# Kernel optimization log

Measured on AMD Instinct MI355X. Metric: run time of the kernel, lower is better.

## Reference

```python
import jax, jax.numpy as jnp
import numpy as np

EMBED_DIM = 1024
NUM_HEADS = 16
HEAD_DIM = EMBED_DIM // NUM_HEADS
MAX_LEN = 1000  # default in RelativePositionalEncoding
B, T = 4, 1024


def setup_inputs() -> dict:
    key = jax.random.key(0)
    ks = jax.random.split(key, 12)
    s = 0.02
    d = EMBED_DIM
    return {
        "query": jax.random.normal(ks[0], (B, T, d), jnp.float32),
        "key": jax.random.normal(ks[1], (B, T, d), jnp.float32),
        "value": jax.random.normal(ks[2], (B, T, d), jnp.float32),
        "Wq": jax.random.normal(ks[3], (d, d), jnp.float32) * s,
        "bq": jnp.zeros((d,), jnp.float32),
        "Wk": jax.random.normal(ks[4], (d, d), jnp.float32) * s,
        "bk": jnp.zeros((d,), jnp.float32),
        "Wv": jax.random.normal(ks[5], (d, d), jnp.float32) * s,
        "bv": jnp.zeros((d,), jnp.float32),
        "Wo": jax.random.normal(ks[6], (d, d), jnp.float32) * s,
        "bo": jnp.zeros((d,), jnp.float32),
        "rel_emb": jax.random.normal(ks[7], (2 * MAX_LEN - 1, HEAD_DIM), jnp.float32) * s,
    }


def reference(query, key, value, Wq, bq, Wk, bk, Wv, bv, Wo, bo, rel_emb):
    Bq, Tq, C = query.shape
    H, hd = NUM_HEADS, HEAD_DIM
    # projections -> [B, H, T, hd]
    q = (query @ Wq.T + bq).reshape(Bq, Tq, H, hd).transpose(0, 2, 1, 3)
    k = (key @ Wk.T + bk).reshape(Bq, Tq, H, hd).transpose(0, 2, 1, 3)
    v = (value @ Wv.T + bv).reshape(Bq, Tq, H, hd).transpose(0, 2, 1, 3)
    # content scores [B, H, T, T]
    attn_scores = jnp.einsum('bhtd,bhsd->bhts', q, k)
    # relative positional embedding gather: E[t, s] = rel_emb[clamp(s - t + max_len - 1)]
    pos = jnp.arange(Tq)
    idx = jnp.clip(pos[None, :] - pos[:, None] + MAX_LEN - 1, 0, 2 * MAX_LEN - 2)
    E = rel_emb[idx]  # [T, T, hd]
    # NOTE: original uses raw (unprojected) query reshaped into heads for rel-pos scores
    rpe_q = query.transpose(1, 0, 2).reshape(Tq, Bq * H, hd)  # [T, B*H, hd]
    rpe = jnp.einsum('tnd,tsd->nts', rpe_q, E).reshape(Bq, H, Tq, Tq)
    # faithful to original: divide by scale = hd**-0.5 (i.e. multiply by sqrt(hd))
    scale = hd ** (-0.5)
    attn = (attn_scores + rpe) / scale
    attn_weights = jax.nn.softmax(attn, axis=-1)
    out = jnp.einsum('bhts,bhsd->bhtd', attn_weights, v)
    out = out.transpose(0, 2, 1, 3).reshape(Bq, Tq, C)
    return out @ Wo.T + bo
```

## Files before the change

### kernel.cpp

```cpp
#include <hip/hip_runtime.h>
#include <math.h>

typedef _Float16 h16;
typedef __attribute__((ext_vector_type(8))) _Float16 half8;
typedef __attribute__((ext_vector_type(4))) float f32x4;

#define MFMA16(a, b, c) __builtin_amdgcn_mfma_f32_16x16x32_f16((a), (b), (c), 0, 0, 0)

__device__ __forceinline__ float ex2(float x) {
  return __builtin_amdgcn_exp2f(x);
}

template <bool A_F16>
__device__ __forceinline__ void gemm_body(const void* __restrict__ Ap,
                                          const float* __restrict__ Bt,
                                          const float* __restrict__ bias,
                                          void* __restrict__ outp, int mode) {
  __shared__ alignas(16) h16 As[128 * 32];
  __shared__ alignas(16) h16 Bs[128 * 32];
  const int tid = threadIdx.x;
  const int wave = tid >> 6;
  const int lane = tid & 63;
  const int wm = wave >> 1, wn = wave & 1;
  const int tm0 = blockIdx.x * 128, tn0 = blockIdx.y * 128;
  const int lrow = lane & 15;
  const int kq = lane >> 4;

  f32x4 acc[4][4];
#pragma unroll
  for (int i = 0; i < 4; ++i)
#pragma unroll
    for (int j = 0; j < 4; ++j) acc[i][j] = (f32x4){0.f, 0.f, 0.f, 0.f};

  for (int k0 = 0; k0 < 1024; k0 += 32) {
    __syncthreads();
#pragma unroll
    for (int rep = 0; rep < 2; ++rep) {
      const int idx = rep * 256 + tid;
      const int row = idx >> 2;
      const int c8 = (idx & 3) * 8;
      if (A_F16) {
        *(half8*)(As + row * 32 + c8) = *(const half8*)(
            (const h16*)Ap + (size_t)(tm0 + row) * 1024 + k0 + c8);
      } else {
        const float* ga =
            (const float*)Ap + (size_t)(tm0 + row) * 1024 + k0 + c8;
        float4 f0 = *(const float4*)ga;
        float4 f1 = *(const float4*)(ga + 4);
        half8 s;
        s[0] = (h16)f0.x; s[1] = (h16)f0.y; s[2] = (h16)f0.z; s[3] = (h16)f0.w;
        s[4] = (h16)f1.x; s[5] = (h16)f1.y; s[6] = (h16)f1.z; s[7] = (h16)f1.w;
        *(half8*)(As + row * 32 + c8) = s;
      }
      const float* gb = Bt + (size_t)(tn0 + row) * 1024 + k0 + c8;
      float4 g0 = *(const float4*)gb;
      float4 g1 = *(const float4*)(gb + 4);
      half8 sb;
      sb[0] = (h16)g0.x; sb[1] = (h16)g0.y; sb[2] = (h16)g0.z; sb[3] = (h16)g0.w;
      sb[4] = (h16)g1.x; sb[5] = (h16)g1.y; sb[6] = (h16)g1.z; sb[7] = (h16)g1.w;
      *(half8*)(Bs + row * 32 + c8) = sb;
    }
    __syncthreads();
    half8 af[4], bf[4];
#pragma unroll
    for (int i = 0; i < 4; ++i)
      af[i] = *(const half8*)(As + (wm * 64 + i * 16 + lrow) * 32 + kq * 8);
#pragma unroll
    for (int j = 0; j < 4; ++j)
      bf[j] = *(const half8*)(Bs + (wn * 64 + j * 16 + lrow) * 32 + kq * 8);
#pragma unroll
    for (int i = 0; i < 4; ++i)
#pragma unroll
      for (int j = 0; j < 4; ++j) acc[i][j] = MFMA16(af[i], bf[j], acc[i][j]);
  }

#pragma unroll
  for (int j = 0; j < 4; ++j) {
    const int n = tn0 + wn * 64 + j * 16 + lrow;
    const float bval = bias[n];
#pragma unroll
    for (int i = 0; i < 4; ++i) {
      const int rowb = wm * 64 + i * 16 + kq * 4;
#pragma unroll
      for (int r = 0; r < 4; ++r) {
        const int m = tm0 + rowb + r;
        const float val = acc[i][j][r] + bval;
        if (mode == 0) {
          const int b = m >> 10, t = m & 1023, hh = n >> 6, d = n & 63;
          ((h16*)outp)[((size_t)((b << 4) + hh) << 16) + (t << 6) + d] =
              (h16)val;
        } else if (mode == 1) {
          const int b = m >> 10, t = m & 1023, hh = n >> 6, d = n & 63;
          ((h16*)outp)[(((size_t)((b << 4) + hh) * 64 + d) << 10) + t] =
              (h16)val;
        } else {
          ((float*)outp)[(size_t)m * 1024 + n] = val;
        }
      }
    }
  }
}

__global__ __launch_bounds__(256) void qkv_gemm(
    const float* q_in, const float* k_in, const float* v_in, const float* Wq,
    const float* Wk, const float* Wv, const float* bq, const float* bk,
    const float* bv, h16* q16, h16* k16, h16* vt16) {
  const int z = blockIdx.z;
  const float* A = (z == 0) ? q_in : (z == 1) ? k_in : v_in;
  const float* Bt = (z == 0) ? Wq : (z == 1) ? Wk : Wv;
  const float* bias = (z == 0) ? bq : (z == 1) ? bk : bv;
  void* outp = (z == 0) ? (void*)q16 : (z == 1) ? (void*)k16 : (void*)vt16;
  gemm_body<false>(A, Bt, bias, outp, (z == 2) ? 1 : 0);
}

__global__ __launch_bounds__(256) void out_gemm(const h16* A, const float* Wo,
                                                const float* bo, float* out) {
  gemm_body<true>(A, Wo, bo, out, 2);
}

__global__ __launch_bounds__(256) void prep(const float* __restrict__ rel,
                                            h16* __restrict__ relb) {
  const int j = blockIdx.x * 256 + threadIdx.x;
  if (j < 2000 * 64) {
    const int row = j >> 6;
    relb[j] = (h16)(row < 1999 ? rel[j] : 0.f);
  }
}

__global__ __launch_bounds__(256, 4) void attn_mfma(
    const h16* __restrict__ q16, const h16* __restrict__ k16,
    const h16* __restrict__ vt16, const float* __restrict__ qraw,
    const h16* __restrict__ relb, h16* __restrict__ ao) {
  __shared__ alignas(16) char smem[40960];
  h16* const Kh = (h16*)smem;
  h16* const Rl = (h16*)(smem + 8192);
  h16* const VtS = (h16*)(smem + 24576);
  h16* const Ps = (h16*)(smem + 32768);
  h16* const Gs = (h16*)smem;

  const int bid = blockIdx.x;
  const int ttile = bid & 15;
  const int bh = bid >> 4;
  const int b = bh >> 4, h = bh & 15;
  const int t0 = ttile << 6;
  const int tid = threadIdx.x;
  const int w = tid >> 6;
  const int lane = tid & 63;
  const int l15 = lane & 15;
  const int kq = lane >> 4;

  const int tq = t0 + w * 16 + l15;
  const size_t qoff = ((size_t)bh * 1024 + tq) * 64 + kq * 8;
  half8 aq[2], arq[2];
#pragma unroll
  for (int ks = 0; ks < 2; ++ks) {
    aq[ks] = *(const half8*)(q16 + qoff + ks * 32);
    const float* rp =
        qraw + ((size_t)(b * 1024 + tq)) * 1024 + h * 64 + kq * 8 + ks * 32;
    float4 r0 = *(const float4*)rp;
    float4 r1 = *(const float4*)(rp + 4);
    half8 a;
    a[0] = (h16)r0.x; a[1] = (h16)r0.y; a[2] = (h16)r0.z; a[3] = (h16)r0.w;
    a[4] = (h16)r1.x; a[5] = (h16)r1.y; a[6] = (h16)r1.z; a[7] = (h16)r1.w;
    arq[ks] = a;
  }

  float m2[4], ls[4];
  f32x4 O[4];
#pragma unroll
  for (int r = 0; r < 4; ++r) {
    m2[r] = -1e30f;
    ls[r] = 0.f;
  }
#pragma unroll
  for (int db = 0; db < 4; ++db) O[db] = (f32x4){0.f, 0.f, 0.f, 0.f};

  const int gbase = w * 2176;
  const int trow = w * 16 + kq * 4;

  for (int s0 = 0; s0 < 1024; s0 += 64) {
    __syncthreads();
    for (int i = tid; i < 512; i += 256) {
      const int row = i >> 3, c = i & 7;
      *(half8*)(Kh + row * 64 + ((c ^ (row & 7)) << 3)) = *(const half8*)(
          k16 + ((size_t)(bh * 1024 + s0 + row)) * 64 + c * 8);
    }
    for (int i = tid; i < 512; i += 256) {
      const int row = i >> 3, c = i & 7;
      *(half8*)(VtS + row * 64 + ((c ^ (row & 7)) << 3)) = *(const half8*)(
          vt16 + ((size_t)bh * 64 + row) * 1024 + s0 + c * 8);
    }
    const int base = s0 - t0 + 999 - 63;
    for (int i = tid; i < 1024; i += 256) {
      const int row = i >> 3, c = i & 7;
      int ridx = base + row;
      ridx = ridx < 0 ? 0 : (ridx > 1998 ? 1998 : ridx);
      *(half8*)(Rl + row * 64 + ((c ^ (row & 7)) << 3)) =
          *(const half8*)(relb + (size_t)ridx * 64 + c * 8);
    }
    __syncthreads();

    f32x4 S[4];
#pragma unroll
    for (int ns = 0; ns < 4; ++ns) {
      f32x4 s = (f32x4){0.f, 0.f, 0.f, 0.f};
      const int kr = ns * 16 + l15;
#pragma unroll
      for (int ks = 0; ks < 2; ++ks) {
        const int c = ((ks * 4 + kq) ^ (kr & 7)) << 3;
        s = MFMA16(aq[ks], *(const half8*)(Kh + kr * 64 + c), s);
      }
      S[ns] = s;
    }

    f32x4 G[5];
#pragma unroll
    for (int gi = 0; gi < 5; ++gi) {
      f32x4 g = (f32x4){0.f, 0.f, 0.f, 0.f};
      const int ur = (3 - w + gi) * 16 + l15;
#pragma unroll
      for (int ks = 0; ks < 2; ++ks) {
        const int c = ((ks * 4 + kq) ^ (ur & 7)) << 3;
        g = MFMA16(arq[ks], *(const half8*)(Rl + ur * 64 + c), g);
      }
      G[gi] = g;
    }
    __syncthreads();

#pragma unroll
    for (int gi = 0; gi < 5; ++gi) {
      const int uc = (3 - w + gi) * 16 + l15;
#pragma unroll
      for (int r = 0; r < 4; ++r)
        Gs[gbase + (kq * 4 + r) * 136 + uc] = (h16)G[gi][r];
    }

    const float SC = 11.54156032711170727f;
#pragma unroll
    for (int ns = 0; ns < 4; ++ns) {
      const int sl = ns * 16 + l15;
#pragma unroll
      for (int r = 0; r < 4; ++r) {
        const int u = sl - (trow + r) + 63;
        const float g = (float)Gs[gbase + (kq * 4 + r) * 136 + u];
        S[ns][r] = (S[ns][r] + g) * SC;
      }
    }

#pragma unroll
    for (int r = 0; r < 4; ++r) {
      float mx = fmaxf(fmaxf(S[0][r], S[1][r]), fmaxf(S[2][r], S[3][r]));
      mx = fmaxf(mx, __shfl_xor(mx, 1));
      mx = fmaxf(mx, __shfl_xor(mx, 2));
      mx = fmaxf(mx, __shfl_xor(mx, 4));
      mx = fmaxf(mx, __shfl_xor(mx, 8));
      const float nm = fmaxf(m2[r], mx);
      const float al = ex2(m2[r] - nm);
      m2[r] = nm;
      const int t = trow + r;
      float rs = 0.f;
#pragma unroll
      for (int ns = 0; ns < 4; ++ns) {
        const float p = ex2(S[ns][r] - nm);
        rs += p;
        const int sl = ns * 16 + l15;
        Ps[t * 64 + (((sl >> 3) ^ (t & 7)) << 3) + (sl & 7)] = (h16)p;
      }
      rs += __shfl_xor(rs, 1);
      rs += __shfl_xor(rs, 2);
      rs += __shfl_xor(rs, 4);
      rs += __shfl_xor(rs, 8);
      ls[r] = ls[r] * al + rs;
      O[0][r] *= al;
      O[1][r] *= al;
      O[2][r] *= al;
      O[3][r] *= al;
    }

    const int tp = w * 16 + l15;
#pragma unroll
    for (int ks = 0; ks < 2; ++ks) {
      const int ca = ((ks * 4 + kq) ^ (tp & 7)) << 3;
      half8 pa = *(const half8*)(Ps + tp * 64 + ca);
#pragma unroll
      for (int db = 0; db < 4; ++db) {
        const int vr = db * 16 + l15;
        const int cb = ((ks * 4 + kq) ^ (vr & 7)) << 3;
        O[db] = MFMA16(pa, *(const half8*)(VtS + vr * 64 + cb), O[db]);
      }
    }
  }

#pragma unroll
  for (int r = 0; r < 4; ++r) {
    const float inv = 1.f / ls[r];
    const int t = t0 + trow + r;
    h16* op = ao + ((size_t)(b * 1024 + t)) * 1024 + h * 64;
#pragma unroll
    for (int db = 0; db < 4; ++db) op[db * 16 + l15] = (h16)(O[db][r] * inv);
  }
}

extern "C" void kernel_launch(void* const* d_in, const int* in_sizes, int n_in,
                              void* d_out, int out_size, void* d_ws,
                              size_t ws_size, hipStream_t stream) {
  const float* query = (const float*)d_in[0];
  const float* key = (const float*)d_in[1];
  const float* value = (const float*)d_in[2];
  const float* Wq = (const float*)d_in[3];
  const float* bq = (const float*)d_in[4];
  const float* Wk = (const float*)d_in[5];
  const float* bk = (const float*)d_in[6];
  const float* Wv = (const float*)d_in[7];
  const float* bv = (const float*)d_in[8];
  const float* Wo = (const float*)d_in[9];
  const float* bo = (const float*)d_in[10];
  const float* rel = (const float*)d_in[11];

  char* ws = (char*)d_ws;
  h16* q16 = (h16*)ws;
  h16* k16 = (h16*)(ws + ((size_t)8 << 20));
  h16* vt16 = (h16*)(ws + ((size_t)16 << 20));
  h16* ao = (h16*)(ws + ((size_t)24 << 20));
  h16* relb = (h16*)(ws + ((size_t)32 << 20));
  float* out = (float*)d_out;

  prep<<<500, 256, 0, stream>>>(rel, relb);
  qkv_gemm<<<dim3(32, 8, 3), 256, 0, stream>>>(query, key, value, Wq, Wk, Wv,
                                               bq, bk, bv, q16, k16, vt16);
  attn_mfma<<<1024, 256, 0, stream>>>(q16, k16, vt16, query, relb, ao);
  out_gemm<<<dim3(32, 8), 256, 0, stream>>>(ao, Wo, bo, out);
}
```

Measured before the change: 311.5 us.

## Pre-convert inputs to fp16, use direct global-to-LDS loads, shuffle rel-pos scores

A single convert kernel now casts the activations, weights and rel_emb to fp16 once, up front. The GEMMs can then load tiles straight into LDS with global_load_lds instead of converting fp32 values per tile. The attention kernel reads the pre-converted raw query and redistributes the relative-position scores with cross-lane shuffles instead of an LDS round-trip and an extra barrier. The output GEMM switches to 64-row tiles so it launches more blocks. The cost is an extra full pass over the inputs to write fp16 copies, plus more workspace.

```diff
diff --git a/kernel.cpp b/kernel.cpp
--- a/kernel.cpp
+++ b/kernel.cpp
@@ -2,20 +2,64 @@
 #include <math.h>
 
 typedef _Float16 h16;
+typedef __attribute__((ext_vector_type(4))) _Float16 half4;
 typedef __attribute__((ext_vector_type(8))) _Float16 half8;
 typedef __attribute__((ext_vector_type(4))) float f32x4;
 
+#define AS1 __attribute__((address_space(1)))
+#define AS3 __attribute__((address_space(3)))
 #define MFMA16(a, b, c) __builtin_amdgcn_mfma_f32_16x16x32_f16((a), (b), (c), 0, 0, 0)
 
 __device__ __forceinline__ float ex2(float x) {
   return __builtin_amdgcn_exp2f(x);
 }
 
-template <bool A_F16>
-__device__ __forceinline__ void gemm_body(const void* __restrict__ Ap,
-                                          const float* __restrict__ Bt,
-                                          const float* __restrict__ bias,
-                                          void* __restrict__ outp, int mode) {
+__global__ __launch_bounds__(256) void convert(
+    const float* __restrict__ q, const float* __restrict__ k,
+    const float* __restrict__ v, const float* __restrict__ Wq,
+    const float* __restrict__ Wk, const float* __restrict__ Wv,
+    const float* __restrict__ Wo, const float* __restrict__ rel, h16* q16c,
+    h16* k16c, h16* v16c, h16* Wq16, h16* Wk16, h16* Wv16, h16* Wo16,
+    h16* relb) {
+  const int i = blockIdx.x * 256 + threadIdx.x;
+  if (i >= 4226304) return;
+  const float* src;
+  h16* dst;
+  int off;
+  if (i < 1048576) {
+    src = q; dst = q16c; off = i;
+  } else if (i < 2097152) {
+    src = k; dst = k16c; off = i - 1048576;
+  } else if (i < 3145728) {
+    src = v; dst = v16c; off = i - 2097152;
+  } else if (i < 3407872) {
+    src = Wq; dst = Wq16; off = i - 3145728;
+  } else if (i < 3670016) {
+    src = Wk; dst = Wk16; off = i - 3407872;
+  } else if (i < 3932160) {
+    src = Wv; dst = Wv16; off = i - 3670016;
+  } else if (i < 4194304) {
+    src = Wo; dst = Wo16; off = i - 3932160;
+  } else {
+    off = i - 4194304;
+    half4 hv = (half4){(h16)0.f, (h16)0.f, (h16)0.f, (h16)0.f};
+    if (off < 31984) {
+      float4 f = *(const float4*)(rel + (size_t)off * 4);
+      hv = (half4){(h16)f.x, (h16)f.y, (h16)f.z, (h16)f.w};
+    }
+    *(half4*)(relb + (size_t)off * 4) = hv;
+    return;
+  }
+  float4 f = *(const float4*)(src + (size_t)off * 4);
+  *(half4*)(dst + (size_t)off * 4) =
+      (half4){(h16)f.x, (h16)f.y, (h16)f.z, (h16)f.w};
+}
+
+template <int MODE>
+__device__ __forceinline__ void gemm128_body(const h16* __restrict__ A,
+                                             const h16* __restrict__ Bt,
+                                             const float* __restrict__ bias,
+                                             h16* __restrict__ outp) {
   __shared__ alignas(16) h16 As[128 * 32];
   __shared__ alignas(16) h16 Bs[128 * 32];
   const int tid = threadIdx.x;
@@ -25,6 +69,8 @@
   const int tm0 = blockIdx.x * 128, tn0 = blockIdx.y * 128;
   const int lrow = lane & 15;
   const int kq = lane >> 4;
+  const int srow = lane >> 2;
+  const int scol = (lane & 3) * 8;
 
   f32x4 acc[4][4];
 #pragma unroll
@@ -36,29 +82,14 @@
     __syncthreads();
 #pragma unroll
     for (int rep = 0; rep < 2; ++rep) {
-      const int idx = rep * 256 + tid;
-      const int row = idx >> 2;
-      const int c8 = (idx & 3) * 8;
-      if (A_F16) {
-        *(half8*)(As + row * 32 + c8) = *(const half8*)(
-            (const h16*)Ap + (size_t)(tm0 + row) * 1024 + k0 + c8);
-      } else {
-        const float* ga =
-            (const float*)Ap + (size_t)(tm0 + row) * 1024 + k0 + c8;
-        float4 f0 = *(const float4*)ga;
-        float4 f1 = *(const float4*)(ga + 4);
-        half8 s;
-        s[0] = (h16)f0.x; s[1] = (h16)f0.y; s[2] = (h16)f0.z; s[3] = (h16)f0.w;
-        s[4] = (h16)f1.x; s[5] = (h16)f1.y; s[6] = (h16)f1.z; s[7] = (h16)f1.w;
-        *(half8*)(As + row * 32 + c8) = s;
-      }
-      const float* gb = Bt + (size_t)(tn0 + row) * 1024 + k0 + c8;
-      float4 g0 = *(const float4*)gb;
-      float4 g1 = *(const float4*)(gb + 4);
-      half8 sb;
-      sb[0] = (h16)g0.x; sb[1] = (h16)g0.y; sb[2] = (h16)g0.z; sb[3] = (h16)g0.w;
-      sb[4] = (h16)g1.x; sb[5] = (h16)g1.y; sb[6] = (h16)g1.z; sb[7] = (h16)g1.w;
-      *(half8*)(Bs + row * 32 + c8) = sb;
+      const int cw = wave * 2 + rep;
+      const int row = cw * 16 + srow;
+      __builtin_amdgcn_global_load_lds(
+          (const AS1 void*)(A + (size_t)(tm0 + row) * 1024 + k0 + scol),
+          (AS3 void*)(As + cw * 512), 16, 0, 0);
+      __builtin_amdgcn_global_load_lds(
+          (const AS1 void*)(Bt + (size_t)(tn0 + row) * 1024 + k0 + scol),
+          (AS3 void*)(Bs + cw * 512), 16, 0, 0);
     }
     __syncthreads();
     half8 af[4], bf[4];
@@ -85,16 +116,11 @@
       for (int r = 0; r < 4; ++r) {
         const int m = tm0 + rowb + r;
         const float val = acc[i][j][r] + bval;
-        if (mode == 0) {
-          const int b = m >> 10, t = m & 1023, hh = n >> 6, d = n & 63;
-          ((h16*)outp)[((size_t)((b << 4) + hh) << 16) + (t << 6) + d] =
-              (h16)val;
-        } else if (mode == 1) {
-          const int b = m >> 10, t = m & 1023, hh = n >> 6, d = n & 63;
-          ((h16*)outp)[(((size_t)((b << 4) + hh) * 64 + d) << 10) + t] =
-              (h16)val;
+        const int b = m >> 10, t = m & 1023, hh = n >> 6, d = n & 63;
+        if (MODE == 0) {
+          outp[((size_t)((b << 4) + hh) << 16) + (t << 6) + d] = (h16)val;
         } else {
-          ((float*)outp)[(size_t)m * 1024 + n] = val;
+          outp[(((size_t)((b << 4) + hh) * 64 + d) << 10) + t] = (h16)val;
         }
       }
     }
@@ -102,41 +128,95 @@
 }
 
 __global__ __launch_bounds__(256) void qkv_gemm(
-    const float* q_in, const float* k_in, const float* v_in, const float* Wq,
-    const float* Wk, const float* Wv, const float* bq, const float* bk,
+    const h16* q16c, const h16* k16c, const h16* v16c, const h16* Wq16,
+    const h16* Wk16, const h16* Wv16, const float* bq, const float* bk,
     const float* bv, h16* q16, h16* k16, h16* vt16) {
   const int z = blockIdx.z;
-  const float* A = (z == 0) ? q_in : (z == 1) ? k_in : v_in;
-  const float* Bt = (z == 0) ? Wq : (z == 1) ? Wk : Wv;
+  const h16* A = (z == 0) ? q16c : (z == 1) ? k16c : v16c;
+  const h16* Bt = (z == 0) ? Wq16 : (z == 1) ? Wk16 : Wv16;
   const float* bias = (z == 0) ? bq : (z == 1) ? bk : bv;
-  void* outp = (z == 0) ? (void*)q16 : (z == 1) ? (void*)k16 : (void*)vt16;
-  gemm_body<false>(A, Bt, bias, outp, (z == 2) ? 1 : 0);
-}
-
-__global__ __launch_bounds__(256) void out_gemm(const h16* A, const float* Wo,
-                                                const float* bo, float* out) {
-  gemm_body<true>(A, Wo, bo, out, 2);
-}
-
-__global__ __launch_bounds__(256) void prep(const float* __restrict__ rel,
-                                            h16* __restrict__ relb) {
-  const int j = blockIdx.x * 256 + threadIdx.x;
-  if (j < 2000 * 64) {
-    const int row = j >> 6;
-    relb[j] = (h16)(row < 1999 ? rel[j] : 0.f);
+  if (z == 2)
+    gemm128_body<1>(A, Bt, bias, vt16);
+  else
+    gemm128_body<0>(A, Bt, bias, (z == 0) ? q16 : k16);
+}
+
+__global__ __launch_bounds__(256) void out_gemm(const h16* __restrict__ A,
+                                                const h16* __restrict__ Bt,
+                                                const float* __restrict__ bo,
+                                                float* __restrict__ out) {
+  __shared__ alignas(16) h16 As[64 * 32];
+  __shared__ alignas(16) h16 Bs[128 * 32];
+  const int tid = threadIdx.x;
+  const int wave = tid >> 6;
+  const int lane = tid & 63;
+  const int wm = wave >> 1, wn = wave & 1;
+  const int tm0 = blockIdx.x * 64, tn0 = blockIdx.y * 128;
+  const int lrow = lane & 15;
+  const int kq = lane >> 4;
+  const int srow = lane >> 2;
+  const int scol = (lane & 3) * 8;
+
+  f32x4 acc[2][4];
+#pragma unroll
+  for (int i = 0; i < 2; ++i)
+#pragma unroll
+    for (int j = 0; j < 4; ++j) acc[i][j] = (f32x4){0.f, 0.f, 0.f, 0.f};
+
+  for (int k0 = 0; k0 < 1024; k0 += 32) {
+    __syncthreads();
+    {
+      const int row = wave * 16 + srow;
+      __builtin_amdgcn_global_load_lds(
+          (const AS1 void*)(A + (size_t)(tm0 + row) * 1024 + k0 + scol),
+          (AS3 void*)(As + wave * 512), 16, 0, 0);
+    }
+#pragma unroll
+    for (int rep = 0; rep < 2; ++rep) {
+      const int cw = wave * 2 + rep;
+      const int row = cw * 16 + srow;
+      __builtin_amdgcn_global_load_lds(
+          (const AS1 void*)(Bt + (size_t)(tn0 + row) * 1024 + k0 + scol),
+          (AS3 void*)(Bs + cw * 512), 16, 0, 0);
+    }
+    __syncthreads();
+    half8 af[2], bf[4];
+#pragma unroll
+    for (int i = 0; i < 2; ++i)
+      af[i] = *(const half8*)(As + (wm * 32 + i * 16 + lrow) * 32 + kq * 8);
+#pragma unroll
+    for (int j = 0; j < 4; ++j)
+      bf[j] = *(const half8*)(Bs + (wn * 64 + j * 16 + lrow) * 32 + kq * 8);
+#pragma unroll
+    for (int i = 0; i < 2; ++i)
+#pragma unroll
+      for (int j = 0; j < 4; ++j) acc[i][j] = MFMA16(af[i], bf[j], acc[i][j]);
+  }
+
+#pragma unroll
+  for (int j = 0; j < 4; ++j) {
+    const int n = tn0 + wn * 64 + j * 16 + lrow;
+    const float bval = bo[n];
+#pragma unroll
+    for (int i = 0; i < 2; ++i) {
+      const int rowb = wm * 32 + i * 16 + kq * 4;
+#pragma unroll
+      for (int r = 0; r < 4; ++r) {
+        const int m = tm0 + rowb + r;
+        out[(size_t)m * 1024 + n] = acc[i][j][r] + bval;
+      }
+    }
   }
 }
 
 __global__ __launch_bounds__(256, 4) void attn_mfma(
     const h16* __restrict__ q16, const h16* __restrict__ k16,
-    const h16* __restrict__ vt16, const float* __restrict__ qraw,
+    const h16* __restrict__ vt16, const h16* __restrict__ q16c,
     const h16* __restrict__ relb, h16* __restrict__ ao) {
-  __shared__ alignas(16) char smem[40960];
-  h16* const Kh = (h16*)smem;
-  h16* const Rl = (h16*)(smem + 8192);
-  h16* const VtS = (h16*)(smem + 24576);
-  h16* const Ps = (h16*)(smem + 32768);
-  h16* const Gs = (h16*)smem;
+  __shared__ alignas(16) h16 Kh[4096];
+  __shared__ alignas(16) h16 Rl[8192];
+  __shared__ alignas(16) h16 VtS[4096];
+  __shared__ alignas(16) h16 Ps[4096];
 
   const int bid = blockIdx.x;
   const int ttile = bid & 15;
@@ -150,19 +230,13 @@
   const int kq = lane >> 4;
 
   const int tq = t0 + w * 16 + l15;
-  const size_t qoff = ((size_t)bh * 1024 + tq) * 64 + kq * 8;
   half8 aq[2], arq[2];
 #pragma unroll
   for (int ks = 0; ks < 2; ++ks) {
-    aq[ks] = *(const half8*)(q16 + qoff + ks * 32);
-    const float* rp =
-        qraw + ((size_t)(b * 1024 + tq)) * 1024 + h * 64 + kq * 8 + ks * 32;
-    float4 r0 = *(const float4*)rp;
-    float4 r1 = *(const float4*)(rp + 4);
-    half8 a;
-    a[0] = (h16)r0.x; a[1] = (h16)r0.y; a[2] = (h16)r0.z; a[3] = (h16)r0.w;
-    a[4] = (h16)r1.x; a[5] = (h16)r1.y; a[6] = (h16)r1.z; a[7] = (h16)r1.w;
-    arq[ks] = a;
+    aq[ks] =
+        *(const half8*)(q16 + ((size_t)bh * 1024 + tq) * 64 + kq * 8 + ks * 32);
+    arq[ks] = *(const half8*)(q16c + ((size_t)(b * 1024 + tq)) * 1024 + h * 64 +
+                              kq * 8 + ks * 32);
   }
 
   float m2[4], ls[4];
@@ -175,7 +249,6 @@
 #pragma unroll
   for (int db = 0; db < 4; ++db) O[db] = (f32x4){0.f, 0.f, 0.f, 0.f};
 
-  const int gbase = w * 2176;
   const int trow = w * 16 + kq * 4;
 
   for (int s0 = 0; s0 < 1024; s0 += 64) {
@@ -225,24 +298,19 @@
       }
       G[gi] = g;
     }
-    __syncthreads();
-
-#pragma unroll
-    for (int gi = 0; gi < 5; ++gi) {
-      const int uc = (3 - w + gi) * 16 + l15;
-#pragma unroll
-      for (int r = 0; r < 4; ++r)
-        Gs[gbase + (kq * 4 + r) * 136 + uc] = (h16)G[gi][r];
-    }
 
     const float SC = 11.54156032711170727f;
+    const int C0 = 63 - w * 16 - kq * 4;
 #pragma unroll
     for (int ns = 0; ns < 4; ++ns) {
-      const int sl = ns * 16 + l15;
 #pragma unroll
       for (int r = 0; r < 4; ++r) {
-        const int u = sl - (trow + r) + 63;
-        const float g = (float)Gs[gbase + (kq * 4 + r) * 136 + u];
+        const int u = l15 + C0 + ns * 16 - r;
+        const int src = (kq << 4) | (u & 15);
+        const int gsel = (u >> 4) + w - 3;
+        const float v0 = __shfl(G[ns][r], src, 64);
+        const float v1 = __shfl(G[(ns + 1) <= 4 ? (ns + 1) : 4][r], src, 64);
+        const float g = (gsel == ns) ? v0 : v1;
         S[ns][r] = (S[ns][r] + g) * SC;
       }
     }
@@ -318,16 +386,26 @@
   const float* rel = (const float*)d_in[11];
 
   char* ws = (char*)d_ws;
-  h16* q16 = (h16*)ws;
-  h16* k16 = (h16*)(ws + ((size_t)8 << 20));
-  h16* vt16 = (h16*)(ws + ((size_t)16 << 20));
-  h16* ao = (h16*)(ws + ((size_t)24 << 20));
-  h16* relb = (h16*)(ws + ((size_t)32 << 20));
+  h16* q16c = (h16*)ws;
+  h16* k16c = (h16*)(ws + ((size_t)8 << 20));
+  h16* v16c = (h16*)(ws + ((size_t)16 << 20));
+  h16* Wq16 = (h16*)(ws + ((size_t)24 << 20));
+  h16* Wk16 = (h16*)(ws + ((size_t)26 << 20));
+  h16* Wv16 = (h16*)(ws + ((size_t)28 << 20));
+  h16* Wo16 = (h16*)(ws + ((size_t)30 << 20));
+  h16* q16 = (h16*)(ws + ((size_t)32 << 20));
+  h16* k16 = (h16*)(ws + ((size_t)40 << 20));
+  h16* vt16 = (h16*)(ws + ((size_t)48 << 20));
+  h16* relb = (h16*)(ws + ((size_t)56 << 20));
+  h16* ao = k16c;
   float* out = (float*)d_out;
 
-  prep<<<500, 256, 0, stream>>>(rel, relb);
-  qkv_gemm<<<dim3(32, 8, 3), 256, 0, stream>>>(query, key, value, Wq, Wk, Wv,
-                                               bq, bk, bv, q16, k16, vt16);
-  attn_mfma<<<1024, 256, 0, stream>>>(q16, k16, vt16, query, relb, ao);
-  out_gemm<<<dim3(32, 8), 256, 0, stream>>>(ao, Wo, bo, out);
-}
+  convert<<<16509, 256, 0, stream>>>(query, key, value, Wq, Wk, Wv, Wo, rel,
+                                     q16c, k16c, v16c, Wq16, Wk16, Wv16, Wo16,
+                                     relb);
+  qkv_gemm<<<dim3(32, 8, 3), 256, 0, stream>>>(q16c, k16c, v16c, Wq16, Wk16,
+                                               Wv16, bq, bk, bv, q16, k16,
+                                               vt16);
+  attn_mfma<<<1024, 256, 0, stream>>>(q16, k16, vt16, q16c, relb, ao);
+  out_gemm<<<dim3(64, 8), 256, 0, stream>>>(ao, Wo16, bo, out);
+}
```

Result: faster. 288.2 us (-7.5%).
